# Kernel tuning notes

Hardware: AMD Instinct MI355X
Metric: run time of the kernel (lower is better)

## Reference

```python
import jax, jax.numpy as jnp
import numpy as np

N = 50000      # nodes
E = 800000     # edges
D = 256        # embed_dim
H = 8          # num_heads
HD = D // H    # head_dim = 32
F = 4 * D      # feedforward_dim = 1024
SCALE = D ** -0.5  # note: module scales by embed_dim**-0.5, not head_dim
EPS = 1e-5


def setup_inputs() -> dict:
    key = jax.random.key(0)
    ks = jax.random.split(key, 10)
    x = jax.random.normal(ks[0], (N, D), dtype=jnp.float32)
    edge_indices = jax.random.randint(ks[1], (2, E), 0, N, dtype=jnp.int32)
    s = 0.02
    return {
        "x": x,
        "edge_indices": edge_indices,
        "w_qkv": jax.random.normal(ks[2], (D, 3 * D), dtype=jnp.float32) * s,
        "b_qkv": jnp.zeros((3 * D,), dtype=jnp.float32),
        "ln1_g": jnp.ones((D,), dtype=jnp.float32),
        "ln1_b": jnp.zeros((D,), dtype=jnp.float32),
        "ln2_g": jnp.ones((D,), dtype=jnp.float32),
        "ln2_b": jnp.zeros((D,), dtype=jnp.float32),
        "w1": jax.random.normal(ks[3], (D, F), dtype=jnp.float32) * s,
        "b1": jnp.zeros((F,), dtype=jnp.float32),
        "w2": jax.random.normal(ks[4], (F, D), dtype=jnp.float32) * s,
        "b2": jnp.zeros((D,), dtype=jnp.float32),
    }


def _layer_norm(x, g, b):
    m = jnp.mean(x, axis=-1, keepdims=True)
    v = jnp.mean((x - m) ** 2, axis=-1, keepdims=True)
    return (x - m) * jax.lax.rsqrt(v + EPS) * g + b


def _self_attention(x, edge_indices, w_qkv, b_qkv):
    qkv = (x @ w_qkv + b_qkv).reshape(N, H, 3 * HD)
    q, k, v = qkv[..., :HD], qkv[..., HD:2 * HD], qkv[..., 2 * HD:]
    rows, cols = edge_indices[0], edge_indices[1]
    # per-edge, per-head attention logits: [E, H]
    alpha = jnp.einsum('ehd,ehd->eh', q[rows], k[cols]) * SCALE
    # sparse softmax over each row (destination node) segment
    m = jax.ops.segment_max(alpha, rows, num_segments=N)       # [N, H]
    ea = jnp.exp(alpha - m[rows])                              # [E, H]
    denom = jax.ops.segment_sum(ea, rows, num_segments=N)      # [N, H]
    w = ea / denom[rows]                                       # [E, H]
    # per-head SpMM: out[r] += w_e * v[c]  -> [N, H, HD]
    out = jax.ops.segment_sum(w[:, :, None] * v[cols], rows, num_segments=N)
    return out.reshape(N, D)


def reference(x, edge_indices, w_qkv, b_qkv, ln1_g, ln1_b, ln2_g, ln2_b, w1, b1, w2, b2):
    # post-norm (norm_first=False), dropout=0
    x = _layer_norm(x + _self_attention(x, edge_indices, w_qkv, b_qkv), ln1_g, ln1_b)
    ffn = jax.nn.relu(x @ w1 + b1) @ w2 + b2
    x = _layer_norm(x + ffn, ln2_g, ln2_b)
    return x
```

## Files before the change

### kernel.cpp

```cpp
#include <hip/hip_runtime.h>
#include <hip/hip_bf16.h>

#define N_NODES 50000
#define E_EDGES 800000
#define D_MODEL 256
#define H_HEADS 8
#define HDIM    32
#define F_FFN   1024
#define ATT_SCALE 0.0625f
#define LN_EPS  1e-5f
#define NB_SCAN 196

typedef __attribute__((ext_vector_type(8))) short bf16x8;
typedef __attribute__((ext_vector_type(4))) float f32x4;

__device__ __forceinline__ float bf2f(__hip_bfloat16 v) { return __bfloat162float(v); }
__device__ __forceinline__ __hip_bfloat16 f2bf(float v) { return __float2bfloat16(v); }
__device__ __forceinline__ unsigned short bfbits(float f) {
    __hip_bfloat16 h = __float2bfloat16(f);
    return *reinterpret_cast<unsigned short*>(&h);
}
__device__ __forceinline__ unsigned char f2fp8(float v) {
    return (unsigned char)(__builtin_amdgcn_cvt_pk_fp8_f32(v, v, 0, false) & 0xff);
}

__device__ __forceinline__ float4 load_bf16x4(const __hip_bfloat16* p) {
    uint2 u = *reinterpret_cast<const uint2*>(p);
    float4 r;
    r.x = __uint_as_float(u.x << 16);
    r.y = __uint_as_float(u.x & 0xFFFF0000u);
    r.z = __uint_as_float(u.y << 16);
    r.w = __uint_as_float(u.y & 0xFFFF0000u);
    return r;
}

__device__ __forceinline__ void load_lds16(const void* g, void* l) {
    __builtin_amdgcn_global_load_lds(
        (const __attribute__((address_space(1))) unsigned*)g,
        (__attribute__((address_space(3))) unsigned*)l, 16, 0, 0);
}

#define PREP_X   3200000
#define PREP_WQ  (768 * 256)
#define PREP_W1  (1024 * 256)
#define PREP_W2  (256 * 1024)
#define PREP_TOT (PREP_X + PREP_WQ + PREP_W1 + PREP_W2 + N_NODES)
__global__ void prep_kernel(const float* __restrict__ x, unsigned short* __restrict__ xb,
                            const float* __restrict__ wq, __hip_bfloat16* __restrict__ wtq,
                            const float* __restrict__ w1, __hip_bfloat16* __restrict__ wt1,
                            const float* __restrict__ w2, __hip_bfloat16* __restrict__ wt2,
                            unsigned* __restrict__ counts, unsigned* __restrict__ cursor) {
    int i = blockIdx.x * blockDim.x + threadIdx.x;
    if (i < PREP_X) {
        float4 v = reinterpret_cast<const float4*>(x)[i];
        ushort4 o;
        o.x = bfbits(v.x); o.y = bfbits(v.y); o.z = bfbits(v.z); o.w = bfbits(v.w);
        reinterpret_cast<ushort4*>(xb)[i] = o;
        return;
    }
    i -= PREP_X;
    if (i < PREP_WQ) {
        int n = i >> 8, k = i & 255;
        wtq[i] = f2bf(wq[(size_t)k * 768 + n]);
        return;
    }
    i -= PREP_WQ;
    if (i < PREP_W1) {
        int n = i >> 8, k = i & 255;
        wt1[i] = f2bf(w1[(size_t)k * 1024 + n]);
        return;
    }
    i -= PREP_W1;
    if (i < PREP_W2) {
        int n = i >> 10, k = i & 1023;
        wt2[i] = f2bf(w2[(size_t)k * 256 + n]);
        return;
    }
    i -= PREP_W2;
    if (i < N_NODES) { counts[i] = 0u; cursor[i] = 0u; }
}

template<bool RELU, bool OUT_BF16, bool SPLIT>
__global__ __launch_bounds__(256)
void mfma_gemm(const __hip_bfloat16* __restrict__ A,
               const __hip_bfloat16* __restrict__ Wt,
               const float* __restrict__ bias,
               void* __restrict__ outp,
               __hip_bfloat16* __restrict__ qb,
               unsigned char* __restrict__ kv8,
               int M, int Ncols, int K) {
    __shared__ short Al[128 * 32];
    __shared__ short Bl[128 * 32];
    const int t = threadIdx.x;
    const int wave = t >> 6, lane = t & 63;
    const int m0 = blockIdx.y * 128, n0 = blockIdx.x * 128;
    const int wr = wave >> 1, wc = wave & 1;

    const int srow = lane >> 2;
    const int skp  = (lane & 3) ^ ((lane >> 3) & 3);
    const int c0 = wave * 2;
    int ar0 = m0 + c0 * 16 + srow;      if (ar0 >= M) ar0 = M - 1;
    int ar1 = m0 + c0 * 16 + 16 + srow; if (ar1 >= M) ar1 = M - 1;
    const __hip_bfloat16* ga0 = A + (size_t)ar0 * K + skp * 8;
    const __hip_bfloat16* ga1 = A + (size_t)ar1 * K + skp * 8;
    const __hip_bfloat16* gb0 = Wt + (size_t)(n0 + c0 * 16 + srow) * K + skp * 8;
    const __hip_bfloat16* gb1 = Wt + (size_t)(n0 + c0 * 16 + 16 + srow) * K + skp * 8;
    short* la0 = &Al[c0 * 512];
    short* la1 = &Al[c0 * 512 + 512];
    short* lb0 = &Bl[c0 * 512];
    short* lb1 = &Bl[c0 * 512 + 512];

    const int lh = lane & 15, q = lane >> 4;
    const int qs = q ^ ((lane >> 1) & 3);
    const short* fa = &Al[(wr * 64 + lh) * 32 + qs * 8];
    const short* fb = &Bl[(wc * 64 + lh) * 32 + qs * 8];

    f32x4 acc[4][4] = {};

    for (int k0 = 0; k0 < K; k0 += 32) {
        load_lds16(ga0, la0);
        load_lds16(ga1, la1);
        load_lds16(gb0, lb0);
        load_lds16(gb1, lb1);
        ga0 += 32; ga1 += 32; gb0 += 32; gb1 += 32;
        __syncthreads();

        bf16x8 af[4], bfr[4];
#pragma unroll
        for (int i = 0; i < 4; i++) {
            af[i]  = *reinterpret_cast<const bf16x8*>(fa + i * 16 * 32);
            bfr[i] = *reinterpret_cast<const bf16x8*>(fb + i * 16 * 32);
        }
#pragma unroll
        for (int mi = 0; mi < 4; mi++)
#pragma unroll
            for (int nj = 0; nj < 4; nj++)
                acc[mi][nj] = __builtin_amdgcn_mfma_f32_16x16x32_bf16(
                    af[mi], bfr[nj], acc[mi][nj], 0, 0, 0);
        __syncthreads();
    }

    const int gnbase = n0 + wc * 64 + lh;
    float bv[4];
#pragma unroll
    for (int nj = 0; nj < 4; nj++) bv[nj] = bias[gnbase + nj * 16];

#pragma unroll
    for (int mi = 0; mi < 4; mi++) {
        int gmb = m0 + wr * 64 + mi * 16 + q * 4;
#pragma unroll
        for (int r = 0; r < 4; r++) {
            int gm = gmb + r;
            if (gm >= M) continue;
#pragma unroll
            for (int nj = 0; nj < 4; nj++) {
                int gn = gnbase + nj * 16;
                float v = acc[mi][nj][r] + bv[nj];
                if (RELU) v = fmaxf(v, 0.f);
                if (SPLIT) {
                    int h  = gn / 96;
                    int rr = gn - h * 96;
                    if (rr < 32) {
                        qb[(size_t)gm * 256 + h * 32 + rr] = f2bf(v);
                    } else {
                        int d   = h * 32 + (rr < 64 ? rr - 32 : rr - 64);
                        int off = (d >> 2) * 8 + (d & 3) + (rr < 64 ? 0 : 4);
                        kv8[(size_t)gm * 512 + off] = f2fp8(v);
                    }
                } else if (OUT_BF16) {
                    ((__hip_bfloat16*)outp)[(size_t)gm * Ncols + gn] = f2bf(v);
                } else {
                    ((float*)outp)[(size_t)gm * Ncols + gn] = v;
                }
            }
        }
    }
}

__global__ __launch_bounds__(512)
void ffn2_ln_kernel(const __hip_bfloat16* __restrict__ A,
                    const __hip_bfloat16* __restrict__ Wt,
                    const float* __restrict__ bias,
                    const __hip_bfloat16* __restrict__ resid,
                    const float* __restrict__ g, const float* __restrict__ bb,
                    float* __restrict__ out, int M) {
    __shared__ short Al[64 * 32];
    __shared__ short Bl[256 * 32];
    const int t = threadIdx.x;
    const int wave = t >> 6, lane = t & 63;
    const int m0 = blockIdx.x * 64;
    const int wr = wave >> 2, wc = wave & 3;

    const int srow = lane >> 2;
    const int skp  = (lane & 3) ^ ((lane >> 3) & 3);

    const __hip_bfloat16* gsrc0; short* ldst0;
    const __hip_bfloat16* gsrc1; short* ldst1;
    const __hip_bfloat16* gsrc2 = A; short* ldst2 = Al;
    {
#define STAGE_INIT(GS, LD, C)                                            \
        if ((C) < 4) {                                                   \
            int r_ = m0 + (C) * 16 + srow; if (r_ >= M) r_ = M - 1;      \
            GS = A + (size_t)r_ * 1024 + skp * 8;                        \
            LD = &Al[(C) * 512];                                         \
        } else {                                                         \
            GS = Wt + (size_t)(((C) - 4) * 16 + srow) * 1024 + skp * 8;  \
            LD = &Bl[((C) - 4) * 512];                                   \
        }
        STAGE_INIT(gsrc0, ldst0, wave)
        STAGE_INIT(gsrc1, ldst1, wave + 8)
        if (wave < 4) { STAGE_INIT(gsrc2, ldst2, wave + 16) }
#undef STAGE_INIT
    }

    const int lh = lane & 15, q = lane >> 4;
    const int qs = q ^ ((lane >> 1) & 3);
    const short* fa = &Al[(wr * 32 + lh) * 32 + qs * 8];
    const short* fb = &Bl[(wc * 64 + lh) * 32 + qs * 8];

    f32x4 acc[2][4] = {};

    for (int k0 = 0; k0 < 1024; k0 += 32) {
        load_lds16(gsrc0, ldst0);
        load_lds16(gsrc1, ldst1);
        if (wave < 4) load_lds16(gsrc2, ldst2);
        gsrc0 += 32; gsrc1 += 32; gsrc2 += 32;
        __syncthreads();

        bf16x8 af[2], bfr[4];
#pragma unroll
        for (int i = 0; i < 2; i++)
            af[i]  = *reinterpret_cast<const bf16x8*>(fa + i * 16 * 32);
#pragma unroll
        for (int i = 0; i < 4; i++)
            bfr[i] = *reinterpret_cast<const bf16x8*>(fb + i * 16 * 32);
#pragma unroll
        for (int mi = 0; mi < 2; mi++)
#pragma unroll
            for (int nj = 0; nj < 4; nj++)
                acc[mi][nj] = __builtin_amdgcn_mfma_f32_16x16x32_bf16(
                    af[mi], bfr[nj], acc[mi][nj], 0, 0, 0);
        __syncthreads();
    }

    const int colbase = wc * 64 + lh;
    float bv[4], gv[4], bbv[4];
#pragma unroll
    for (int nj = 0; nj < 4; nj++) {
        bv[nj]  = bias[colbase + nj * 16];
        gv[nj]  = g[colbase + nj * 16];
        bbv[nj] = bb[colbase + nj * 16];
    }

    float ps[2][4], pq[2][4];
#pragma unroll
    for (int mi = 0; mi < 2; mi++) {
#pragma unroll
        for (int r = 0; r < 4; r++) {
            int gm = m0 + wr * 32 + mi * 16 + q * 4 + r;
            int rgm = (gm < M) ? gm : M - 1;
            float s = 0.f, s2 = 0.f;
#pragma unroll
            for (int nj = 0; nj < 4; nj++) {
                float v = acc[mi][nj][r] + bv[nj]
                        + bf2f(resid[(size_t)rgm * 256 + colbase + nj * 16]);
                acc[mi][nj][r] = v;
                s += v; s2 += v * v;
            }
            ps[mi][r] = s; pq[mi][r] = s2;
        }
    }
#pragma unroll
    for (int off = 1; off <= 8; off <<= 1) {
#pragma unroll
        for (int mi = 0; mi < 2; mi++)
#pragma unroll
            for (int r = 0; r < 4; r++) {
                ps[mi][r] += __shfl_xor(ps[mi][r], off);
                pq[mi][r] += __shfl_xor(pq[mi][r], off);
            }
    }
    float* rs = (float*)Al;
    float* rq = (float*)(Al + 512);
    if (lh == 0) {
#pragma unroll
        for (int mi = 0; mi < 2; mi++)
#pragma unroll
            for (int r = 0; r < 4; r++) {
                int m = wr * 32 + mi * 16 + q * 4 + r;
                rs[m * 4 + wc] = ps[mi][r];
                rq[m * 4 + wc] = pq[mi][r];
            }
    }
    __syncthreads();

#pragma unroll
    for (int mi = 0; mi < 2; mi++) {
#pragma unroll
        for (int r = 0; r < 4; r++) {
            int m = wr * 32 + mi * 16 + q * 4 + r;
            int gm = m0 + m;
            if (gm >= M) continue;
            float4 rsv = *reinterpret_cast<const float4*>(&rs[m * 4]);
            float4 rqv = *reinterpret_cast<const float4*>(&rq[m * 4]);
            float S  = (rsv.x + rsv.y) + (rsv.z + rsv.w);
            float S2 = (rqv.x + rqv.y) + (rqv.z + rqv.w);
            float mean = S * (1.f / (float)D_MODEL);
            float var  = S2 * (1.f / (float)D_MODEL) - mean * mean;
            float inv  = rsqrtf(var + LN_EPS);
#pragma unroll
            for (int nj = 0; nj < 4; nj++)
                out[(size_t)gm * 256 + colbase + nj * 16] =
                    (acc[mi][nj][r] - mean) * inv * gv[nj] + bbv[nj];
        }
    }
}

__global__ void count_kernel(const int* __restrict__ rows, unsigned* __restrict__ counts) {
    int e = blockIdx.x * blockDim.x + threadIdx.x;
    if (e < E_EDGES) atomicAdd(&counts[rows[e]], 1u);
}

__global__ void scan_blk_kernel(const unsigned* __restrict__ counts,
                                unsigned* __restrict__ offs, unsigned* __restrict__ bsum) {
    __shared__ unsigned sh[256];
    int t = threadIdx.x;
    int i = blockIdx.x * 256 + t;
    unsigned v = (i < N_NODES) ? counts[i] : 0u;
    sh[t] = v;
    __syncthreads();
#pragma unroll
    for (int off = 1; off < 256; off <<= 1) {
        unsigned u = (t >= off) ? sh[t - off] : 0u;
        __syncthreads();
        sh[t] += u;
        __syncthreads();
    }
    if (i < N_NODES) offs[i] = sh[t] - v;
    if (t == 255) bsum[blockIdx.x] = sh[255];
}

__global__ void scan_top_kernel(const unsigned* __restrict__ bsum, unsigned* __restrict__ bpre) {
    __shared__ unsigned sh[256];
    int t = threadIdx.x;
    unsigned v = (t < NB_SCAN) ? bsum[t] : 0u;
    sh[t] = v;
    __syncthreads();
#pragma unroll
    for (int off = 1; off < 256; off <<= 1) {
        unsigned u = (t >= off) ? sh[t - off] : 0u;
        __syncthreads();
        sh[t] += u;
        __syncthreads();
    }
    if (t < NB_SCAN) bpre[t] = sh[t] - v;
    if (t == NB_SCAN - 1) bpre[NB_SCAN] = sh[t];
}

__global__ void scan_add_kernel(unsigned* __restrict__ offs, const unsigned* __restrict__ bpre) {
    int i = blockIdx.x * 256 + threadIdx.x;
    if (i < N_NODES) offs[i] += bpre[blockIdx.x];
    if (i == 0) offs[N_NODES] = bpre[NB_SCAN];
}

__global__ void scatter_kernel(const int* __restrict__ rows, const int* __restrict__ cols,
                               const unsigned* __restrict__ offsets, unsigned* __restrict__ cursor,
                               int* __restrict__ scol) {
    int e = blockIdx.x * blockDim.x + threadIdx.x;
    if (e >= E_EDGES) return;
    int r = rows[e];
    unsigned idx = atomicAdd(&cursor[r], 1u);
    scol[offsets[r] + idx] = cols[e];
}

__global__ __launch_bounds__(256)
void att_agg_kernel(const __hip_bfloat16* __restrict__ qb,
                    const unsigned char* __restrict__ kv8,
                    const unsigned* __restrict__ offsets,
                    const int* __restrict__ scol,
                    const float* __restrict__ x,
                    const float* __restrict__ g, const float* __restrict__ bb,
                    __hip_bfloat16* __restrict__ xn) {
    int n = blockIdx.x * 4 + (threadIdx.x >> 6);
    if (n >= N_NODES) return;
    int lam = threadIdx.x & 63;
    unsigned beg = offsets[n], end = offsets[n + 1];

    float4 qf = load_bf16x4(qb + (size_t)n * 256 + lam * 4);
    qf.x *= ATT_SCALE; qf.y *= ATT_SCALE; qf.z *= ATT_SCALE; qf.w *= ATT_SCALE;

    float4 acc = {0.f, 0.f, 0.f, 0.f};
    float l = 0.f;

#define EDGE_BODY(KV, SV, PV)                                                 \
    unsigned klo = (unsigned)(KV), vhi = (unsigned)((KV) >> 32);              \
    auto k01 = __builtin_amdgcn_cvt_pk_f32_fp8((int)klo, false);              \
    auto k23 = __builtin_amdgcn_cvt_pk_f32_fp8((int)klo, true);               \
    float SV = qf.x * k01[0] + qf.y * k01[1] + qf.z * k23[0] + qf.w * k23[1]; \
    SV += __shfl_xor(SV, 1);                                                  \
    SV += __shfl_xor(SV, 2);                                                  \
    SV += __shfl_xor(SV, 4);                                                  \
    float PV = __expf(SV);                                                    \
    auto v01 = __builtin_amdgcn_cvt_pk_f32_fp8((int)vhi, false);              \
    auto v23 = __builtin_amdgcn_cvt_pk_f32_fp8((int)vhi, true);               \
    l += PV;                                                                  \
    acc.x += PV * v01[0]; acc.y += PV * v01[1];                               \
    acc.z += PV * v23[0]; acc.w += PV * v23[1];

    unsigned e = beg;
    for (; e + 4 <= end; e += 4) {
        int c0 = scol[e], c1 = scol[e + 1], c2 = scol[e + 2], c3 = scol[e + 3];
        unsigned long long kv0 = *(const unsigned long long*)(kv8 + (size_t)c0 * 512 + lam * 8);
        unsigned long long kv1 = *(const unsigned long long*)(kv8 + (size_t)c1 * 512 + lam * 8);
        unsigned long long kv2 = *(const unsigned long long*)(kv8 + (size_t)c2 * 512 + lam * 8);
        unsigned long long kv3 = *(const unsigned long long*)(kv8 + (size_t)c3 * 512 + lam * 8);
        { EDGE_BODY(kv0, s0, p0) }
        { EDGE_BODY(kv1, s1, p1) }
        { EDGE_BODY(kv2, s2, p2) }
        { EDGE_BODY(kv3, s3, p3) }
    }
    for (; e < end; e++) {
        int c0 = scol[e];
        unsigned long long kv0 = *(const unsigned long long*)(kv8 + (size_t)c0 * 512 + lam * 8);
        { EDGE_BODY(kv0, s0, p0) }
    }
#undef EDGE_BODY

    float inv_l = (l > 0.f) ? 1.f / l : 0.f;
    float4 xr = reinterpret_cast<const float4*>(x + (size_t)n * D_MODEL)[lam];
    float4 tv;
    tv.x = acc.x * inv_l + xr.x;
    tv.y = acc.y * inv_l + xr.y;
    tv.z = acc.z * inv_l + xr.z;
    tv.w = acc.w * inv_l + xr.w;

    float s  = tv.x + tv.y + tv.z + tv.w;
    float s2 = tv.x * tv.x + tv.y * tv.y + tv.z * tv.z + tv.w * tv.w;
#pragma unroll
    for (int off = 1; off <= 32; off <<= 1) {
        s  += __shfl_xor(s, off);
        s2 += __shfl_xor(s2, off);
    }
    float mean = s * (1.f / (float)D_MODEL);
    float var  = s2 * (1.f / (float)D_MODEL) - mean * mean;
    float inv  = rsqrtf(var + LN_EPS);

    float4 gr = reinterpret_cast<const float4*>(g  + lam * 4)[0];
    float4 br = reinterpret_cast<const float4*>(bb + lam * 4)[0];
    ushort4 o;
    o.x = bfbits((tv.x - mean) * inv * gr.x + br.x);
    o.y = bfbits((tv.y - mean) * inv * gr.y + br.y);
    o.z = bfbits((tv.z - mean) * inv * gr.z + br.z);
    o.w = bfbits((tv.w - mean) * inv * gr.w + br.w);
    reinterpret_cast<ushort4*>(xn + (size_t)n * D_MODEL)[lam] = o;
}

extern "C" void kernel_launch(void* const* d_in, const int* in_sizes, int n_in,
                              void* d_out, int out_size, void* d_ws, size_t ws_size,
                              hipStream_t stream) {
    const float* x     = (const float*)d_in[0];
    const int*   ei    = (const int*)d_in[1];
    const float* w_qkv = (const float*)d_in[2];
    const float* b_qkv = (const float*)d_in[3];
    const float* ln1_g = (const float*)d_in[4];
    const float* ln1_b = (const float*)d_in[5];
    const float* ln2_g = (const float*)d_in[6];
    const float* ln2_b = (const float*)d_in[7];
    const float* w1    = (const float*)d_in[8];
    const float* b1    = (const float*)d_in[9];
    const float* w2    = (const float*)d_in[10];
    const float* b2    = (const float*)d_in[11];
    const int* rows = ei;
    const int* cols = ei + E_EDGES;

    char* ws = (char*)d_ws;
    __hip_bfloat16* qb      = (__hip_bfloat16*)(ws + 0);
    unsigned char*  kv8     = (unsigned char*)(ws + 25600000);
    __hip_bfloat16* hbuf    = (__hip_bfloat16*)(ws + 0);
    __hip_bfloat16* xb      = (__hip_bfloat16*)(ws + 102400000);
    __hip_bfloat16* wtq     = (__hip_bfloat16*)(ws + 128000000);
    __hip_bfloat16* wt1     = (__hip_bfloat16*)(ws + 128400000);
    __hip_bfloat16* wt2     = (__hip_bfloat16*)(ws + 129000000);
    unsigned*       counts  = (unsigned*)(ws + 129600000);
    unsigned*       offsets = (unsigned*)(ws + 129800000);
    unsigned*       cursor  = (unsigned*)(ws + 130000008);
    int*            scol    = (int*)(ws + 130200008);
    unsigned*       bsum    = (unsigned*)(ws + 133400008);
    unsigned*       bpre    = (unsigned*)(ws + 133401032);
    __hip_bfloat16* xn      = (__hip_bfloat16*)(ws + 153600000);

    const int nbM = (N_NODES + 127) / 128;

    prep_kernel<<<(PREP_TOT + 255) / 256, 256, 0, stream>>>(
        x, (unsigned short*)xb, w_qkv, wtq, w1, wt1, w2, wt2, counts, cursor);

    mfma_gemm<false, true, true><<<dim3(768 / 128, nbM), 256, 0, stream>>>(
        xb, wtq, b_qkv, nullptr, qb, kv8, N_NODES, 768, D_MODEL);

    count_kernel<<<(E_EDGES + 255) / 256, 256, 0, stream>>>(rows, counts);
    scan_blk_kernel<<<NB_SCAN, 256, 0, stream>>>(counts, offsets, bsum);
    scan_top_kernel<<<1, 256, 0, stream>>>(bsum, bpre);
    scan_add_kernel<<<NB_SCAN, 256, 0, stream>>>(offsets, bpre);
    scatter_kernel<<<(E_EDGES + 255) / 256, 256, 0, stream>>>(rows, cols, offsets, cursor, scol);

    att_agg_kernel<<<(N_NODES + 3) / 4, 256, 0, stream>>>(qb, kv8, offsets, scol,
                                                          x, ln1_g, ln1_b, xn);

    mfma_gemm<true, true, false><<<dim3(F_FFN / 128, nbM), 256, 0, stream>>>(
        xn, wt1, b1, hbuf, nullptr, nullptr, N_NODES, F_FFN, D_MODEL);

    ffn2_ln_kernel<<<(N_NODES + 63) / 64, 512, 0, stream>>>(hbuf, wt2, b2, xn, ln2_g, ln2_b,
                                                            (float*)d_out, N_NODES);
}
```

Measured before the change: 460.0 us.

## Vectorize GEMM epilogues via permuted weights, XCD-aware block remap, double-buffer FFN2

Permutes the columns of the QKV and FFN1 weights and biases during prep so each lane holds four adjacent output features. This lets the epilogue issue packed 8-byte bf16 stores and packed 4-byte fp8 stores instead of scalar writes. GEMM workgroup ids are remapped so consecutive tiles land on the same XCD, for better L2 reuse. The FFN2+LayerNorm kernel gains a double-buffered LDS pipeline to overlap global-to-LDS loads with MFMA. In exchange it uses more LDS and adds index arithmetic in prep.

```diff
diff --git a/kernel.cpp b/kernel.cpp
--- a/kernel.cpp
+++ b/kernel.cpp
@@ -20,9 +20,6 @@
     __hip_bfloat16 h = __float2bfloat16(f);
     return *reinterpret_cast<unsigned short*>(&h);
 }
-__device__ __forceinline__ unsigned char f2fp8(float v) {
-    return (unsigned char)(__builtin_amdgcn_cvt_pk_fp8_f32(v, v, 0, false) & 0xff);
-}
 
 __device__ __forceinline__ float4 load_bf16x4(const __hip_bfloat16* p) {
     uint2 u = *reinterpret_cast<const uint2*>(p);
@@ -40,15 +37,20 @@
         (__attribute__((address_space(3))) unsigned*)l, 16, 0, 0);
 }
 
+
 #define PREP_X   3200000
 #define PREP_WQ  (768 * 256)
 #define PREP_W1  (1024 * 256)
 #define PREP_W2  (256 * 1024)
-#define PREP_TOT (PREP_X + PREP_WQ + PREP_W1 + PREP_W2 + N_NODES)
+#define PREP_BQ  768
+#define PREP_B1  1024
+#define PREP_TOT (PREP_X + PREP_WQ + PREP_W1 + PREP_W2 + PREP_BQ + PREP_B1 + N_NODES)
 __global__ void prep_kernel(const float* __restrict__ x, unsigned short* __restrict__ xb,
                             const float* __restrict__ wq, __hip_bfloat16* __restrict__ wtq,
                             const float* __restrict__ w1, __hip_bfloat16* __restrict__ wt1,
                             const float* __restrict__ w2, __hip_bfloat16* __restrict__ wt2,
+                            const float* __restrict__ bq, float* __restrict__ bqp,
+                            const float* __restrict__ b1, float* __restrict__ b1p,
                             unsigned* __restrict__ counts, unsigned* __restrict__ cursor) {
     int i = blockIdx.x * blockDim.x + threadIdx.x;
     if (i < PREP_X) {
@@ -61,13 +63,17 @@
     i -= PREP_X;
     if (i < PREP_WQ) {
         int n = i >> 8, k = i & 255;
-        wtq[i] = f2bf(wq[(size_t)k * 768 + n]);
+        int s = n >> 8, prel = n & 255;
+        int d = (prel & 192) + ((prel & 15) << 2) + ((prel >> 4) & 3);
+        int co = (d >> 5) * 96 + s * 32 + (d & 31);
+        wtq[i] = f2bf(wq[(size_t)k * 768 + co]);
         return;
     }
     i -= PREP_WQ;
     if (i < PREP_W1) {
         int n = i >> 8, k = i & 255;
-        wt1[i] = f2bf(w1[(size_t)k * 1024 + n]);
+        int f = (n & ~63) + ((n & 15) << 2) + ((n >> 4) & 3);
+        wt1[i] = f2bf(w1[(size_t)k * 1024 + f]);
         return;
     }
     i -= PREP_W1;
@@ -77,15 +83,28 @@
         return;
     }
     i -= PREP_W2;
+    if (i < PREP_BQ) {
+        int s = i >> 8, prel = i & 255;
+        int d = (prel & 192) + ((prel & 15) << 2) + ((prel >> 4) & 3);
+        bqp[i] = bq[(d >> 5) * 96 + s * 32 + (d & 31)];
+        return;
+    }
+    i -= PREP_BQ;
+    if (i < PREP_B1) {
+        int f = (i & ~63) + ((i & 15) << 2) + ((i >> 4) & 3);
+        b1p[i] = b1[f];
+        return;
+    }
+    i -= PREP_B1;
     if (i < N_NODES) { counts[i] = 0u; cursor[i] = 0u; }
 }
 
-template<bool RELU, bool OUT_BF16, bool SPLIT>
+template<bool RELU, int EPI>
 __global__ __launch_bounds__(256)
 void mfma_gemm(const __hip_bfloat16* __restrict__ A,
                const __hip_bfloat16* __restrict__ Wt,
                const float* __restrict__ bias,
-               void* __restrict__ outp,
+               __hip_bfloat16* __restrict__ outp,
                __hip_bfloat16* __restrict__ qb,
                unsigned char* __restrict__ kv8,
                int M, int Ncols, int K) {
@@ -93,7 +112,16 @@
     __shared__ short Bl[128 * 32];
     const int t = threadIdx.x;
     const int wave = t >> 6, lane = t & 63;
-    const int m0 = blockIdx.y * 128, n0 = blockIdx.x * 128;
+
+    unsigned flat = blockIdx.y * gridDim.x + blockIdx.x;
+    unsigned nwg = gridDim.x * gridDim.y;
+    unsigned q8 = nwg >> 3, r8 = nwg & 7;
+    unsigned xcd = flat & 7, pos = flat >> 3;
+    unsigned wg = (xcd < r8) ? (xcd * (q8 + 1) + pos)
+                             : (r8 * (q8 + 1) + (xcd - r8) * q8 + pos);
+    const int m0 = (int)(wg / gridDim.x) * 128;
+    const int n0 = (int)(wg % gridDim.x) * 128;
+
     const int wr = wave >> 1, wc = wave & 1;
 
     const int srow = lane >> 2;
@@ -140,38 +168,58 @@
         __syncthreads();
     }
 
-    const int gnbase = n0 + wc * 64 + lh;
+    const int B = n0 + wc * 64;
+    const int gnbase = B + lh;
     float bv[4];
 #pragma unroll
     for (int nj = 0; nj < 4; nj++) bv[nj] = bias[gnbase + nj * 16];
 
-#pragma unroll
-    for (int mi = 0; mi < 4; mi++) {
-        int gmb = m0 + wr * 64 + mi * 16 + q * 4;
-#pragma unroll
-        for (int r = 0; r < 4; r++) {
-            int gm = gmb + r;
-            if (gm >= M) continue;
-#pragma unroll
-            for (int nj = 0; nj < 4; nj++) {
-                int gn = gnbase + nj * 16;
-                float v = acc[mi][nj][r] + bv[nj];
-                if (RELU) v = fmaxf(v, 0.f);
-                if (SPLIT) {
-                    int h  = gn / 96;
-                    int rr = gn - h * 96;
-                    if (rr < 32) {
-                        qb[(size_t)gm * 256 + h * 32 + rr] = f2bf(v);
-                    } else {
-                        int d   = h * 32 + (rr < 64 ? rr - 32 : rr - 64);
-                        int off = (d >> 2) * 8 + (d & 3) + (rr < 64 ? 0 : 4);
-                        kv8[(size_t)gm * 512 + off] = f2fp8(v);
-                    }
-                } else if (OUT_BF16) {
-                    ((__hip_bfloat16*)outp)[(size_t)gm * Ncols + gn] = f2bf(v);
+    if (EPI == 0) {
+        const int sec = B >> 8;
+        const int c = ((B & 255) >> 6) * 16 + lh;
+#pragma unroll
+        for (int mi = 0; mi < 4; mi++) {
+            int gmb = m0 + wr * 64 + mi * 16 + q * 4;
+#pragma unroll
+            for (int r = 0; r < 4; r++) {
+                int gm = gmb + r;
+                if (gm >= M) continue;
+                float v0 = acc[mi][0][r] + bv[0];
+                float v1 = acc[mi][1][r] + bv[1];
+                float v2 = acc[mi][2][r] + bv[2];
+                float v3 = acc[mi][3][r] + bv[3];
+                if (sec == 0) {
+                    ushort4 o;
+                    o.x = bfbits(v0); o.y = bfbits(v1); o.z = bfbits(v2); o.w = bfbits(v3);
+                    *reinterpret_cast<ushort4*>(qb + (size_t)gm * 256 + c * 4) = o;
                 } else {
-                    ((float*)outp)[(size_t)gm * Ncols + gn] = v;
+                    unsigned u = (unsigned)__builtin_amdgcn_cvt_pk_fp8_f32(v0, v1, 0, false);
+                    u = (unsigned)__builtin_amdgcn_cvt_pk_fp8_f32(v2, v3, (int)u, true);
+                    *reinterpret_cast<unsigned*>(
+                        kv8 + (size_t)gm * 512 + c * 8 + (sec == 1 ? 0 : 4)) = u;
                 }
+            }
+        }
+    } else {
+        const int cb = B + lh * 4;
+#pragma unroll
+        for (int mi = 0; mi < 4; mi++) {
+            int gmb = m0 + wr * 64 + mi * 16 + q * 4;
+#pragma unroll
+            for (int r = 0; r < 4; r++) {
+                int gm = gmb + r;
+                if (gm >= M) continue;
+                float v0 = acc[mi][0][r] + bv[0];
+                float v1 = acc[mi][1][r] + bv[1];
+                float v2 = acc[mi][2][r] + bv[2];
+                float v3 = acc[mi][3][r] + bv[3];
+                if (RELU) {
+                    v0 = fmaxf(v0, 0.f); v1 = fmaxf(v1, 0.f);
+                    v2 = fmaxf(v2, 0.f); v3 = fmaxf(v3, 0.f);
+                }
+                ushort4 o;
+                o.x = bfbits(v0); o.y = bfbits(v1); o.z = bfbits(v2); o.w = bfbits(v3);
+                *reinterpret_cast<ushort4*>(outp + (size_t)gm * Ncols + cb) = o;
             }
         }
     }
@@ -184,8 +232,7 @@
                     const __hip_bfloat16* __restrict__ resid,
                     const float* __restrict__ g, const float* __restrict__ bb,
                     float* __restrict__ out, int M) {
-    __shared__ short Al[64 * 32];
-    __shared__ short Bl[256 * 32];
+    __shared__ short LDS[2][(64 + 256) * 32];
     const int t = threadIdx.x;
     const int wave = t >> 6, lane = t & 63;
     const int m0 = blockIdx.x * 64;
@@ -194,54 +241,71 @@
     const int srow = lane >> 2;
     const int skp  = (lane & 3) ^ ((lane >> 3) & 3);
 
-    const __hip_bfloat16* gsrc0; short* ldst0;
-    const __hip_bfloat16* gsrc1; short* ldst1;
-    const __hip_bfloat16* gsrc2 = A; short* ldst2 = Al;
+    const __hip_bfloat16* gsrc0; int loff0;
+    const __hip_bfloat16* gsrc1; int loff1;
+    const __hip_bfloat16* gsrc2; int loff2;
     {
-#define STAGE_INIT(GS, LD, C)                                            \
+#define STAGE_INIT(GS, LO, C)                                            \
         if ((C) < 4) {                                                   \
             int r_ = m0 + (C) * 16 + srow; if (r_ >= M) r_ = M - 1;      \
             GS = A + (size_t)r_ * 1024 + skp * 8;                        \
-            LD = &Al[(C) * 512];                                         \
+            LO = (C) * 512;                                              \
         } else {                                                         \
             GS = Wt + (size_t)(((C) - 4) * 16 + srow) * 1024 + skp * 8;  \
-            LD = &Bl[((C) - 4) * 512];                                   \
+            LO = 2048 + ((C) - 4) * 512;                                 \
         }
-        STAGE_INIT(gsrc0, ldst0, wave)
-        STAGE_INIT(gsrc1, ldst1, wave + 8)
-        if (wave < 4) { STAGE_INIT(gsrc2, ldst2, wave + 16) }
+        STAGE_INIT(gsrc0, loff0, wave)
+        STAGE_INIT(gsrc1, loff1, wave + 8)
+        int c2 = (wave < 4) ? wave + 16 : 16;
+        STAGE_INIT(gsrc2, loff2, c2)
 #undef STAGE_INIT
     }
 
     const int lh = lane & 15, q = lane >> 4;
     const int qs = q ^ ((lane >> 1) & 3);
-    const short* fa = &Al[(wr * 32 + lh) * 32 + qs * 8];
-    const short* fb = &Bl[(wc * 64 + lh) * 32 + qs * 8];
+    const short* fa0 = &LDS[0][(wr * 32 + lh) * 32 + qs * 8];
+    const short* fb0 = &LDS[0][2048 + (wc * 64 + lh) * 32 + qs * 8];
+    const short* fa1 = &LDS[1][(wr * 32 + lh) * 32 + qs * 8];
+    const short* fb1 = &LDS[1][2048 + (wc * 64 + lh) * 32 + qs * 8];
 
     f32x4 acc[2][4] = {};
 
-    for (int k0 = 0; k0 < 1024; k0 += 32) {
-        load_lds16(gsrc0, ldst0);
-        load_lds16(gsrc1, ldst1);
-        if (wave < 4) load_lds16(gsrc2, ldst2);
-        gsrc0 += 32; gsrc1 += 32; gsrc2 += 32;
-        __syncthreads();
-
-        bf16x8 af[2], bfr[4];
-#pragma unroll
-        for (int i = 0; i < 2; i++)
-            af[i]  = *reinterpret_cast<const bf16x8*>(fa + i * 16 * 32);
-#pragma unroll
-        for (int i = 0; i < 4; i++)
-            bfr[i] = *reinterpret_cast<const bf16x8*>(fb + i * 16 * 32);
-#pragma unroll
-        for (int mi = 0; mi < 2; mi++)
-#pragma unroll
-            for (int nj = 0; nj < 4; nj++)
-                acc[mi][nj] = __builtin_amdgcn_mfma_f32_16x16x32_bf16(
-                    af[mi], bfr[nj], acc[mi][nj], 0, 0, 0);
-        __syncthreads();
-    }
+#define FFN2_STAGE(BUF)                                      \
+    load_lds16(gsrc0, &LDS[BUF][loff0]);                     \
+    load_lds16(gsrc1, &LDS[BUF][loff1]);                     \
+    if (wave < 4) load_lds16(gsrc2, &LDS[BUF][loff2]);       \
+    gsrc0 += 32; gsrc1 += 32; gsrc2 += 32;
+
+#define FFN2_STEP(FA, FB)                                                   \
+    {                                                                       \
+        bf16x8 af[2], bfr[4];                                               \
+        _Pragma("unroll")                                                   \
+        for (int i = 0; i < 2; i++)                                         \
+            af[i] = *reinterpret_cast<const bf16x8*>((FA) + i * 16 * 32);   \
+        _Pragma("unroll")                                                   \
+        for (int i = 0; i < 4; i++)                                         \
+            bfr[i] = *reinterpret_cast<const bf16x8*>((FB) + i * 16 * 32);  \
+        _Pragma("unroll")                                                   \
+        for (int mi = 0; mi < 2; mi++)                                      \
+            _Pragma("unroll")                                               \
+            for (int nj = 0; nj < 4; nj++)                                  \
+                acc[mi][nj] = __builtin_amdgcn_mfma_f32_16x16x32_bf16(      \
+                    af[mi], bfr[nj], acc[mi][nj], 0, 0, 0);                 \
+    }
+
+    FFN2_STAGE(0)
+    __syncthreads();
+
+    for (int s = 0; s < 32; s += 2) {
+        FFN2_STAGE(1)
+        FFN2_STEP(fa0, fb0)
+        __syncthreads();
+        if (s < 30) { FFN2_STAGE(0) }
+        FFN2_STEP(fa1, fb1)
+        __syncthreads();
+    }
+#undef FFN2_STAGE
+#undef FFN2_STEP
 
     const int colbase = wc * 64 + lh;
     float bv[4], gv[4], bbv[4];
@@ -280,8 +344,8 @@
                 pq[mi][r] += __shfl_xor(pq[mi][r], off);
             }
     }
-    float* rs = (float*)Al;
-    float* rq = (float*)(Al + 512);
+    float* rs = (float*)(&LDS[0][0]);
+    float* rq = rs + 256;
     if (lh == 0) {
 #pragma unroll
         for (int mi = 0; mi < 2; mi++)
@@ -487,15 +551,18 @@
     int*            scol    = (int*)(ws + 130200008);
     unsigned*       bsum    = (unsigned*)(ws + 133400008);
     unsigned*       bpre    = (unsigned*)(ws + 133401032);
+    float*          bqp     = (float*)(ws + 133500000);
+    float*          b1p     = (float*)(ws + 133510000);
     __hip_bfloat16* xn      = (__hip_bfloat16*)(ws + 153600000);
 
     const int nbM = (N_NODES + 127) / 128;
 
     prep_kernel<<<(PREP_TOT + 255) / 256, 256, 0, stream>>>(
-        x, (unsigned short*)xb, w_qkv, wtq, w1, wt1, w2, wt2, counts, cursor);
-
-    mfma_gemm<false, true, true><<<dim3(768 / 128, nbM), 256, 0, stream>>>(
-        xb, wtq, b_qkv, nullptr, qb, kv8, N_NODES, 768, D_MODEL);
+        x, (unsigned short*)xb, w_qkv, wtq, w1, wt1, w2, wt2,
+        b_qkv, bqp, b1, b1p, counts, cursor);
+
+    mfma_gemm<false, 0><<<dim3(768 / 128, nbM), 256, 0, stream>>>(
+        xb, wtq, bqp, nullptr, qb, kv8, N_NODES, 768, D_MODEL);
 
     count_kernel<<<(E_EDGES + 255) / 256, 256, 0, stream>>>(rows, counts);
     scan_blk_kernel<<<NB_SCAN, 256, 0, stream>>>(counts, offsets, bsum);
@@ -506,8 +573,8 @@
     att_agg_kernel<<<(N_NODES + 3) / 4, 256, 0, stream>>>(qb, kv8, offsets, scol,
                                                           x, ln1_g, ln1_b, xn);
 
-    mfma_gemm<true, true, false><<<dim3(F_FFN / 128, nbM), 256, 0, stream>>>(
-        xn, wt1, b1, hbuf, nullptr, nullptr, N_NODES, F_FFN, D_MODEL);
+    mfma_gemm<true, 1><<<dim3(F_FFN / 128, nbM), 256, 0, stream>>>(
+        xn, wt1, b1p, hbuf, nullptr, nullptr, N_NODES, F_FFN, D_MODEL);
 
     ffn2_ln_kernel<<<(N_NODES + 63) / 64, 512, 0, stream>>>(hbuf, wt2, b2, xn, ln2_g, ln2_b,
                                                             (float*)d_out, N_NODES);
```

Result: faster. 426.5 us (-7.3%).
